# Kernel optimization log

Hardware: AMD Instinct MI355X
Metric: run time of the kernel (lower is better)

## Reference

```python
import jax, jax.numpy as jnp
import numpy as np

N_NODES = 50000
N_EDGES = 1250000
VOCAB = 50000
EMBED = 64
HIDDEN = 64
NUM_REL = 3
N_CLASSES = 2
N_GRAPHS = 512


def setup_inputs() -> dict:
    key = jax.random.key(0)
    ks = jax.random.split(key, 12)
    x = jax.random.randint(ks[0], (N_NODES,), 0, VOCAB, dtype=jnp.int32)
    edge_index = jax.random.randint(ks[1], (2, N_EDGES), 0, N_NODES, dtype=jnp.int32)
    edge_type = jax.random.randint(ks[2], (N_EDGES,), 0, NUM_REL, dtype=jnp.int32)
    batch = jnp.sort(jax.random.randint(ks[3], (N_NODES,), 0, N_GRAPHS, dtype=jnp.int32))
    s = 0.05
    emb = jax.random.normal(ks[4], (VOCAB, EMBED), jnp.float32) * s
    w1_rel = jax.random.normal(ks[5], (NUM_REL, EMBED, HIDDEN), jnp.float32) * s
    w1_root = jax.random.normal(ks[6], (EMBED, HIDDEN), jnp.float32) * s
    b1 = jnp.zeros((HIDDEN,), jnp.float32)
    w2_rel = jax.random.normal(ks[7], (NUM_REL, HIDDEN, HIDDEN), jnp.float32) * s
    w2_root = jax.random.normal(ks[8], (HIDDEN, HIDDEN), jnp.float32) * s
    b2 = jnp.zeros((HIDDEN,), jnp.float32)
    lin_w = jax.random.normal(ks[9], (HIDDEN, N_CLASSES), jnp.float32) * s
    lin_b = jnp.zeros((N_CLASSES,), jnp.float32)
    return {"x": x, "edge_index": edge_index, "edge_type": edge_type, "batch": batch,
            "emb": emb, "w1_rel": w1_rel, "w1_root": w1_root, "b1": b1,
            "w2_rel": w2_rel, "w2_root": w2_root, "b2": b2,
            "lin_w": lin_w, "lin_b": lin_b}


def rgcn_conv(h, src, dst, edge_type, w_rel, w_root, bias):
    # PyG RGCNConv: out = h @ W_root + bias + sum_r mean-aggregated (h_src @ W_r)
    out = h @ w_root + bias
    h_src = h[src]  # [E, F] gather
    for r in range(NUM_REL):
        mask = (edge_type == r).astype(h.dtype)  # [E]
        m = (h_src @ w_rel[r]) * mask[:, None]   # [E, H]
        s = jax.ops.segment_sum(m, dst, num_segments=N_NODES)
        cnt = jax.ops.segment_sum(mask, dst, num_segments=N_NODES)
        out = out + s / jnp.maximum(cnt, 1.0)[:, None]
    return out


def reference(x, edge_index, edge_type, batch, emb, w1_rel, w1_root, b1,
              w2_rel, w2_root, b2, lin_w, lin_b):
    src, dst = edge_index[0], edge_index[1]
    emb_eff = emb.at[0].set(0.0)  # padding_idx=0
    h = emb_eff[x]  # [N, EMBED]
    h = jax.nn.relu(rgcn_conv(h, src, dst, edge_type, w1_rel, w1_root, b1))
    h = jax.nn.relu(rgcn_conv(h, src, dst, edge_type, w2_rel, w2_root, b2))
    # global mean pool over graphs
    sums = jax.ops.segment_sum(h, batch, num_segments=N_GRAPHS)
    cnt = jax.ops.segment_sum(jnp.ones((h.shape[0],), h.dtype), batch, num_segments=N_GRAPHS)
    pooled = sums / jnp.maximum(cnt, 1.0)[:, None]  # [G, HIDDEN]
    return pooled @ lin_w + lin_b  # [G, N_CLASSES]
```

## Files before the change

kernel.cpp:

```cpp
#include <hip/hip_runtime.h>

__global__ __launch_bounds__(256) void embed_kernel(
    const int* __restrict__ x, const float* __restrict__ emb,
    float* __restrict__ h0, int n_nodes)
{
    int t = blockIdx.x * 256 + threadIdx.x;
    if (t >= n_nodes * 16) return;
    int n = t >> 4, q = t & 15;
    int xv = x[n];
    float4 v = {0.f, 0.f, 0.f, 0.f};
    if (xv != 0) v = *(const float4*)(emb + (size_t)xv * 64 + q * 4);
    *(float4*)(h0 + (size_t)n * 64 + q * 4) = v;
}


__global__ __launch_bounds__(256) void bucket_count_kernel(
    const int* __restrict__ ei, int* __restrict__ bucket_count,
    int n_edges, int n_bkt, int per_block)
{
    __shared__ int cnt[512];
    int t = threadIdx.x;
    for (int i = t; i < n_bkt; i += 256) cnt[i] = 0;
    __syncthreads();
    int lo = blockIdx.x * per_block;
    int hi = min(n_edges, lo + per_block);
    for (int e = lo + t; e < hi; e += 256)
        atomicAdd(&cnt[ei[n_edges + e] >> 7], 1);
    __syncthreads();
    for (int i = t; i < n_bkt; i += 256)
        if (cnt[i]) atomicAdd(&bucket_count[i], cnt[i]);
}

__global__ __launch_bounds__(512) void scan_buckets_kernel(
    const int* __restrict__ bucket_count, int* __restrict__ bucket_start,
    int* __restrict__ rowstart, int n_bkt, int n_edges, int n_nodes)
{
    __shared__ int part[512];
    int t = threadIdx.x;
    part[t] = (t < n_bkt) ? bucket_count[t] : 0;
    __syncthreads();
    for (int off = 1; off < 512; off <<= 1) {
        int v = (t >= off) ? part[t - off] : 0;
        __syncthreads();
        part[t] += v;
        __syncthreads();
    }
    if (t == 0) { bucket_start[0] = 0; rowstart[n_nodes] = n_edges; }
    if (t < n_bkt) bucket_start[t + 1] = part[t];
}

__global__ __launch_bounds__(256) void bucket_scatter_kernel(
    const int* __restrict__ ei, const int* __restrict__ et,
    const int* __restrict__ bucket_start, int* __restrict__ bucket_fill,
    int* __restrict__ esort, int n_edges, int n_bkt)
{
    __shared__ int cnt[512], gbase[512], fill2[512];
    const int EPT = 32;
    int t = threadIdx.x;
    int base = blockIdx.x * 256 * EPT;
    for (int i = t; i < n_bkt; i += 256) { cnt[i] = 0; fill2[i] = 0; }
    __syncthreads();
    int pay[EPT], bk[EPT];
#pragma unroll
    for (int i = 0; i < EPT; ++i) {
        int e = base + i * 256 + t;
        bk[i] = -1;
        if (e < n_edges) {
            int s = ei[e], d = ei[n_edges + e], r = et[e];
            int b = d >> 7;
            pay[i] = s | (r << 16) | ((d & 127) << 18);
            bk[i] = b;
            atomicAdd(&cnt[b], 1);
        }
    }
    __syncthreads();
    for (int i = t; i < n_bkt; i += 256)
        if (cnt[i]) gbase[i] = bucket_start[i] + atomicAdd(&bucket_fill[i], cnt[i]);
    __syncthreads();
#pragma unroll
    for (int i = 0; i < EPT; ++i) {
        if (bk[i] >= 0) {
            int pos = gbase[bk[i]] + atomicAdd(&fill2[bk[i]], 1);
            esort[pos] = pay[i];
        }
    }
}

__global__ __launch_bounds__(256) void bucket_sort_kernel(
    const int* __restrict__ bucket_start, int* __restrict__ esort,
    int* __restrict__ scratch, int* __restrict__ rowstart, int n_nodes)
{
    __shared__ int cnt[128], off[128], fill[128], sc[128];
    int t = threadIdx.x, b = blockIdx.x;
    int s = bucket_start[b], e = bucket_start[b + 1];
    if (t < 128) { cnt[t] = 0; fill[t] = 0; }
    __syncthreads();
    int* scr = scratch + (size_t)b * 8192;
    for (int i = s + t; i < e; i += 256) {
        int p = esort[i];
        scr[i - s] = p;
        atomicAdd(&cnt[(p >> 18) & 127], 1);
    }
    __syncthreads();
    if (t < 128) sc[t] = cnt[t];
    __syncthreads();
    for (int o = 1; o < 128; o <<= 1) {
        int v = (t >= o && t < 128) ? sc[t - o] : 0;
        __syncthreads();
        if (t < 128) sc[t] += v;
        __syncthreads();
    }
    if (t < 128) {
        off[t] = sc[t] - cnt[t];
        int d = b * 128 + t;
        if (d < n_nodes) rowstart[d] = s + off[t];
    }
    __syncthreads();
    for (int i = s + t; i < e; i += 256) {
        int p = scr[i - s];
        int dl = (p >> 18) & 127;
        int pos = s + off[dl] + atomicAdd(&fill[dl], 1);
        esort[pos] = p;
    }
}

__global__ __launch_bounds__(256) void agg_kernel(
    const float* __restrict__ hin, const int* __restrict__ rowstart,
    const int* __restrict__ esort, float* __restrict__ means, int n_nodes)
{
    int wid = (blockIdx.x * 256 + threadIdx.x) >> 6;
    int lane = threadIdx.x & 63;
    if (wid >= n_nodes) return;
    int q = lane >> 4;
    int c = lane & 15;
    int s = rowstart[wid], e = rowstart[wid + 1];

    float a0x=0.f,a0y=0.f,a0z=0.f,a0w=0.f, c0=0.f;
    float a1x=0.f,a1y=0.f,a1z=0.f,a1w=0.f, c1=0.f;
    float a2x=0.f,a2y=0.f,a2z=0.f,a2w=0.f, c2=0.f;

    for (int i = s + q; i < e; i += 4) {
        int p = esort[i];
        int src = p & 0xFFFF;
        int r = (p >> 16) & 3;
        float4 v = *(const float4*)(hin + (size_t)src * 64 + c * 4);
        float m0 = (r == 0) ? 1.f : 0.f;
        float m1 = (r == 1) ? 1.f : 0.f;
        float m2 = (r == 2) ? 1.f : 0.f;
        a0x = fmaf(m0, v.x, a0x); a0y = fmaf(m0, v.y, a0y);
        a0z = fmaf(m0, v.z, a0z); a0w = fmaf(m0, v.w, a0w); c0 += m0;
        a1x = fmaf(m1, v.x, a1x); a1y = fmaf(m1, v.y, a1y);
        a1z = fmaf(m1, v.z, a1z); a1w = fmaf(m1, v.w, a1w); c1 += m1;
        a2x = fmaf(m2, v.x, a2x); a2y = fmaf(m2, v.y, a2y);
        a2z = fmaf(m2, v.z, a2z); a2w = fmaf(m2, v.w, a2w); c2 += m2;
    }
#pragma unroll
    for (int off = 16; off < 64; off <<= 1) {
        a0x += __shfl_xor(a0x, off); a0y += __shfl_xor(a0y, off);
        a0z += __shfl_xor(a0z, off); a0w += __shfl_xor(a0w, off);
        a1x += __shfl_xor(a1x, off); a1y += __shfl_xor(a1y, off);
        a1z += __shfl_xor(a1z, off); a1w += __shfl_xor(a1w, off);
        a2x += __shfl_xor(a2x, off); a2y += __shfl_xor(a2y, off);
        a2z += __shfl_xor(a2z, off); a2w += __shfl_xor(a2w, off);
        c0 += __shfl_xor(c0, off); c1 += __shfl_xor(c1, off);
        c2 += __shfl_xor(c2, off);
    }
    if (q < 3) {
        float ax = (q == 0) ? a0x : (q == 1) ? a1x : a2x;
        float ay = (q == 0) ? a0y : (q == 1) ? a1y : a2y;
        float az = (q == 0) ? a0z : (q == 1) ? a1z : a2z;
        float aw = (q == 0) ? a0w : (q == 1) ? a1w : a2w;
        float cc = (q == 0) ? c0  : (q == 1) ? c1  : c2;
        float inv = 1.f / fmaxf(cc, 1.f);
        float4 m;
        m.x = ax * inv; m.y = ay * inv; m.z = az * inv; m.w = aw * inv;
        *(float4*)(means + (size_t)wid * 192 + q * 64 + c * 4) = m;
    }
}

__global__ __launch_bounds__(256) void transform_kernel(
    const float* __restrict__ hin, const float* __restrict__ means,
    const float* __restrict__ wroot, const float* __restrict__ wrel,
    const float* __restrict__ bias, float* __restrict__ hout, int n_nodes)
{
    __shared__ float wsh[256 * 64];
    int t = threadIdx.x;
    {
        const float4* src = (const float4*)wroot;
        float4* dst = (float4*)wsh;
#pragma unroll
        for (int i = 0; i < 4; ++i) dst[t + i * 256] = src[t + i * 256];
        src = (const float4*)wrel;
        dst = (float4*)(wsh + 4096);
#pragma unroll
        for (int i = 0; i < 12; ++i) dst[t + i * 256] = src[t + i * 256];
    }
    __syncthreads();

    int gt = blockIdx.x * 256 + t;
    int g = gt >> 4, q = gt & 15;
    int n0 = g * 4;
    if (n0 >= n_nodes) return;

    float4 b = *(const float4*)(bias + q * 4);
    float acc0x=b.x, acc0y=b.y, acc0z=b.z, acc0w=b.w;
    float acc1x=b.x, acc1y=b.y, acc1z=b.z, acc1w=b.w;
    float acc2x=b.x, acc2y=b.y, acc2z=b.z, acc2w=b.w;
    float acc3x=b.x, acc3y=b.y, acc3z=b.z, acc3w=b.w;

    const float* hv = hin + (size_t)n0 * 64;
#pragma unroll 2
    for (int k4 = 0; k4 < 16; ++k4) {
        float4 va = *(const float4*)(hv +   0 + k4 * 4);
        float4 vb = *(const float4*)(hv +  64 + k4 * 4);
        float4 vc = *(const float4*)(hv + 128 + k4 * 4);
        float4 vd = *(const float4*)(hv + 192 + k4 * 4);
#pragma unroll
        for (int kk = 0; kk < 4; ++kk) {
            float4 w = *(const float4*)(wsh + (k4 * 4 + kk) * 64 + q * 4);
            float a = kk==0?va.x:kk==1?va.y:kk==2?va.z:va.w;
            float bb= kk==0?vb.x:kk==1?vb.y:kk==2?vb.z:vb.w;
            float c = kk==0?vc.x:kk==1?vc.y:kk==2?vc.z:vc.w;
            float d = kk==0?vd.x:kk==1?vd.y:kk==2?vd.z:vd.w;
            acc0x=fmaf(a,w.x,acc0x); acc0y=fmaf(a,w.y,acc0y); acc0z=fmaf(a,w.z,acc0z); acc0w=fmaf(a,w.w,acc0w);
            acc1x=fmaf(bb,w.x,acc1x); acc1y=fmaf(bb,w.y,acc1y); acc1z=fmaf(bb,w.z,acc1z); acc1w=fmaf(bb,w.w,acc1w);
            acc2x=fmaf(c,w.x,acc2x); acc2y=fmaf(c,w.y,acc2y); acc2z=fmaf(c,w.z,acc2z); acc2w=fmaf(c,w.w,acc2w);
            acc3x=fmaf(d,w.x,acc3x); acc3y=fmaf(d,w.y,acc3y); acc3z=fmaf(d,w.z,acc3z); acc3w=fmaf(d,w.w,acc3w);
        }
    }
    const float* mv = means + (size_t)n0 * 192;
#pragma unroll 2
    for (int k4 = 0; k4 < 48; ++k4) {
        float4 va = *(const float4*)(mv +   0 + k4 * 4);
        float4 vb = *(const float4*)(mv + 192 + k4 * 4);
        float4 vc = *(const float4*)(mv + 384 + k4 * 4);
        float4 vd = *(const float4*)(mv + 576 + k4 * 4);
#pragma unroll
        for (int kk = 0; kk < 4; ++kk) {
            float4 w = *(const float4*)(wsh + (64 + k4 * 4 + kk) * 64 + q * 4);
            float a = kk==0?va.x:kk==1?va.y:kk==2?va.z:va.w;
            float bb= kk==0?vb.x:kk==1?vb.y:kk==2?vb.z:vb.w;
            float c = kk==0?vc.x:kk==1?vc.y:kk==2?vc.z:vc.w;
            float d = kk==0?vd.x:kk==1?vd.y:kk==2?vd.z:vd.w;
            acc0x=fmaf(a,w.x,acc0x); acc0y=fmaf(a,w.y,acc0y); acc0z=fmaf(a,w.z,acc0z); acc0w=fmaf(a,w.w,acc0w);
            acc1x=fmaf(bb,w.x,acc1x); acc1y=fmaf(bb,w.y,acc1y); acc1z=fmaf(bb,w.z,acc1z); acc1w=fmaf(bb,w.w,acc1w);
            acc2x=fmaf(c,w.x,acc2x); acc2y=fmaf(c,w.y,acc2y); acc2z=fmaf(c,w.z,acc2z); acc2w=fmaf(c,w.w,acc2w);
            acc3x=fmaf(d,w.x,acc3x); acc3y=fmaf(d,w.y,acc3y); acc3z=fmaf(d,w.z,acc3z); acc3w=fmaf(d,w.w,acc3w);
        }
    }
    float* o = hout + (size_t)n0 * 64 + q * 4;
    float4 r0 = {fmaxf(acc0x,0.f), fmaxf(acc0y,0.f), fmaxf(acc0z,0.f), fmaxf(acc0w,0.f)};
    float4 r1 = {fmaxf(acc1x,0.f), fmaxf(acc1y,0.f), fmaxf(acc1z,0.f), fmaxf(acc1w,0.f)};
    float4 r2 = {fmaxf(acc2x,0.f), fmaxf(acc2y,0.f), fmaxf(acc2z,0.f), fmaxf(acc2w,0.f)};
    float4 r3 = {fmaxf(acc3x,0.f), fmaxf(acc3y,0.f), fmaxf(acc3z,0.f), fmaxf(acc3w,0.f)};
    *(float4*)(o +   0) = r0;
    *(float4*)(o +  64) = r1;
    *(float4*)(o + 128) = r2;
    *(float4*)(o + 192) = r3;
}

__global__ __launch_bounds__(256) void pool_kernel(
    const float* __restrict__ h2, const int* __restrict__ batch,
    const float* __restrict__ linw, const float* __restrict__ linb,
    float* __restrict__ out, int n_nodes, int n_graphs)
{
    int wid = (blockIdx.x * 256 + threadIdx.x) >> 6;
    int lane = threadIdx.x & 63;
    if (wid >= n_graphs) return;
    int g = wid;
    int lo = 0, hi = n_nodes;
    while (lo < hi) { int mid = (lo + hi) >> 1; if (batch[mid] < g) lo = mid + 1; else hi = mid; }
    int s = lo;
    lo = 0; hi = n_nodes;
    while (lo < hi) { int mid = (lo + hi) >> 1; if (batch[mid] < g + 1) lo = mid + 1; else hi = mid; }
    int e = lo;
    float sum = 0.f;
    for (int n = s; n < e; ++n) sum += h2[(size_t)n * 64 + lane];
    float mean = sum / (float)max(e - s, 1);
    float d0 = mean * linw[lane * 2 + 0];
    float d1 = mean * linw[lane * 2 + 1];
    for (int off = 32; off > 0; off >>= 1) {
        d0 += __shfl_down(d0, off);
        d1 += __shfl_down(d1, off);
    }
    if (lane == 0) {
        out[g * 2 + 0] = d0 + linb[0];
        out[g * 2 + 1] = d1 + linb[1];
    }
}

extern "C" void kernel_launch(void* const* d_in, const int* in_sizes, int n_in,
                              void* d_out, int out_size, void* d_ws, size_t ws_size,
                              hipStream_t stream)
{
    const int*   x      = (const int*)d_in[0];
    const int*   ei     = (const int*)d_in[1];
    const int*   et     = (const int*)d_in[2];
    const int*   batch  = (const int*)d_in[3];
    const float* emb    = (const float*)d_in[4];
    const float* w1rel  = (const float*)d_in[5];
    const float* w1root = (const float*)d_in[6];
    const float* b1     = (const float*)d_in[7];
    const float* w2rel  = (const float*)d_in[8];
    const float* w2root = (const float*)d_in[9];
    const float* b2     = (const float*)d_in[10];
    const float* linw   = (const float*)d_in[11];
    const float* linb   = (const float*)d_in[12];
    float* out = (float*)d_out;

    const int N = in_sizes[0];
    const int E = in_sizes[2];
    const int G = out_size / 2;
    const int NBKT = (N + 127) >> 7;

    float* hA        = (float*)d_ws;
    float* hB        = hA + (size_t)N * 64;
    float* means     = hB + (size_t)N * 64;
    int*   esort     = (int*)(means + (size_t)N * 192);
    int*   rowstart  = esort + E;
    int*   bucket_count = rowstart + (N + 1);
    int*   bucket_fill  = bucket_count + 512;
    int*   bucket_start = bucket_fill + 512;

    hipMemsetAsync(bucket_count, 0, (size_t)1024 * sizeof(int), stream);

    embed_kernel<<<(N * 16 + 255) / 256, 256, 0, stream>>>(x, emb, hA, N);

    int per_block = (E + 255) / 256;
    bucket_count_kernel<<<256, 256, 0, stream>>>(ei, bucket_count, E, NBKT, per_block);
    scan_buckets_kernel<<<1, 512, 0, stream>>>(bucket_count, bucket_start, rowstart, NBKT, E, N);
    bucket_scatter_kernel<<<(E + 8191) / 8192, 256, 0, stream>>>(ei, et, bucket_start, bucket_fill, esort, E, NBKT);
    bucket_sort_kernel<<<NBKT, 256, 0, stream>>>(bucket_start, esort, (int*)means, rowstart, N);

    int aggBlocks = (N * 64 + 255) / 256;
    int tfBlocks  = ((N + 3) / 4 * 16 + 255) / 256;
    agg_kernel<<<aggBlocks, 256, 0, stream>>>(hA, rowstart, esort, means, N);
    transform_kernel<<<tfBlocks, 256, 0, stream>>>(hA, means, w1root, w1rel, b1, hB, N);
    agg_kernel<<<aggBlocks, 256, 0, stream>>>(hB, rowstart, esort, means, N);
    transform_kernel<<<tfBlocks, 256, 0, stream>>>(hB, means, w2root, w2rel, b2, hA, N);

    pool_kernel<<<(G * 64 + 255) / 256, 256, 0, stream>>>(hA, batch, linw, linb, out, N, G);
}
```

Baseline: 360.7 us.

## Sort edges by (dst, relation) and tile transform over eight nodes

```diff
diff --git a/kernel.cpp b/kernel.cpp
--- a/kernel.cpp
+++ b/kernel.cpp
@@ -33,7 +33,7 @@
 
 __global__ __launch_bounds__(512) void scan_buckets_kernel(
     const int* __restrict__ bucket_count, int* __restrict__ bucket_start,
-    int* __restrict__ rowstart, int n_bkt, int n_edges, int n_nodes)
+    int* __restrict__ rowstartR, int n_bkt, int n_edges, int n_nodes)
 {
     __shared__ int part[512];
     int t = threadIdx.x;
@@ -45,7 +45,7 @@
         part[t] += v;
         __syncthreads();
     }
-    if (t == 0) { bucket_start[0] = 0; rowstart[n_nodes] = n_edges; }
+    if (t == 0) { bucket_start[0] = 0; rowstartR[4 * n_nodes] = n_edges; }
     if (t < n_bkt) bucket_start[t + 1] = part[t];
 }
 
@@ -88,44 +88,48 @@
 
 __global__ __launch_bounds__(256) void bucket_sort_kernel(
     const int* __restrict__ bucket_start, int* __restrict__ esort,
-    int* __restrict__ scratch, int* __restrict__ rowstart, int n_nodes)
-{
-    __shared__ int cnt[128], off[128], fill[128], sc[128];
+    int* __restrict__ scratch, int* __restrict__ rowstartR, int n_nodes)
+{
+    __shared__ int cnt[512], off[512], fill[512], ps[256];
     int t = threadIdx.x, b = blockIdx.x;
     int s = bucket_start[b], e = bucket_start[b + 1];
-    if (t < 128) { cnt[t] = 0; fill[t] = 0; }
+    cnt[t] = 0; cnt[t + 256] = 0; fill[t] = 0; fill[t + 256] = 0;
     __syncthreads();
     int* scr = scratch + (size_t)b * 8192;
     for (int i = s + t; i < e; i += 256) {
         int p = esort[i];
         scr[i - s] = p;
-        atomicAdd(&cnt[(p >> 18) & 127], 1);
-    }
-    __syncthreads();
-    if (t < 128) sc[t] = cnt[t];
-    __syncthreads();
-    for (int o = 1; o < 128; o <<= 1) {
-        int v = (t >= o && t < 128) ? sc[t - o] : 0;
+        atomicAdd(&cnt[(p >> 16) & 0x1FF], 1);
+    }
+    __syncthreads();
+    int a0 = cnt[2 * t], a1 = cnt[2 * t + 1];
+    ps[t] = a0 + a1;
+    __syncthreads();
+    for (int o = 1; o < 256; o <<= 1) {
+        int v = (t >= o) ? ps[t - o] : 0;
         __syncthreads();
-        if (t < 128) sc[t] += v;
+        ps[t] += v;
         __syncthreads();
     }
-    if (t < 128) {
-        off[t] = sc[t] - cnt[t];
-        int d = b * 128 + t;
-        if (d < n_nodes) rowstart[d] = s + off[t];
-    }
+    int basex = (t > 0) ? ps[t - 1] : 0;
+    off[2 * t] = basex;
+    off[2 * t + 1] = basex + a0;
+    __syncthreads();
+    int d0 = b * 128 + (2 * t >> 2);
+    if (d0 < n_nodes) rowstartR[b * 512 + 2 * t] = s + off[2 * t];
+    int d1 = b * 128 + ((2 * t + 1) >> 2);
+    if (d1 < n_nodes) rowstartR[b * 512 + 2 * t + 1] = s + off[2 * t + 1];
     __syncthreads();
     for (int i = s + t; i < e; i += 256) {
         int p = scr[i - s];
-        int dl = (p >> 18) & 127;
-        int pos = s + off[dl] + atomicAdd(&fill[dl], 1);
+        int bin = (p >> 16) & 0x1FF;
+        int pos = s + off[bin] + atomicAdd(&fill[bin], 1);
         esort[pos] = p;
     }
 }
 
 __global__ __launch_bounds__(256) void agg_kernel(
-    const float* __restrict__ hin, const int* __restrict__ rowstart,
+    const float* __restrict__ hin, const int* __restrict__ rowstartR,
     const int* __restrict__ esort, float* __restrict__ means, int n_nodes)
 {
     int wid = (blockIdx.x * 256 + threadIdx.x) >> 6;
@@ -133,48 +137,27 @@
     if (wid >= n_nodes) return;
     int q = lane >> 4;
     int c = lane & 15;
-    int s = rowstart[wid], e = rowstart[wid + 1];
-
-    float a0x=0.f,a0y=0.f,a0z=0.f,a0w=0.f, c0=0.f;
-    float a1x=0.f,a1y=0.f,a1z=0.f,a1w=0.f, c1=0.f;
-    float a2x=0.f,a2y=0.f,a2z=0.f,a2w=0.f, c2=0.f;
-
-    for (int i = s + q; i < e; i += 4) {
-        int p = esort[i];
-        int src = p & 0xFFFF;
-        int r = (p >> 16) & 3;
-        float4 v = *(const float4*)(hin + (size_t)src * 64 + c * 4);
-        float m0 = (r == 0) ? 1.f : 0.f;
-        float m1 = (r == 1) ? 1.f : 0.f;
-        float m2 = (r == 2) ? 1.f : 0.f;
-        a0x = fmaf(m0, v.x, a0x); a0y = fmaf(m0, v.y, a0y);
-        a0z = fmaf(m0, v.z, a0z); a0w = fmaf(m0, v.w, a0w); c0 += m0;
-        a1x = fmaf(m1, v.x, a1x); a1y = fmaf(m1, v.y, a1y);
-        a1z = fmaf(m1, v.z, a1z); a1w = fmaf(m1, v.w, a1w); c1 += m1;
-        a2x = fmaf(m2, v.x, a2x); a2y = fmaf(m2, v.y, a2y);
-        a2z = fmaf(m2, v.z, a2z); a2w = fmaf(m2, v.w, a2w); c2 += m2;
-    }
-#pragma unroll
-    for (int off = 16; off < 64; off <<= 1) {
-        a0x += __shfl_xor(a0x, off); a0y += __shfl_xor(a0y, off);
-        a0z += __shfl_xor(a0z, off); a0w += __shfl_xor(a0w, off);
-        a1x += __shfl_xor(a1x, off); a1y += __shfl_xor(a1y, off);
-        a1z += __shfl_xor(a1z, off); a1w += __shfl_xor(a1w, off);
-        a2x += __shfl_xor(a2x, off); a2y += __shfl_xor(a2y, off);
-        a2z += __shfl_xor(a2z, off); a2w += __shfl_xor(a2w, off);
-        c0 += __shfl_xor(c0, off); c1 += __shfl_xor(c1, off);
-        c2 += __shfl_xor(c2, off);
-    }
-    if (q < 3) {
-        float ax = (q == 0) ? a0x : (q == 1) ? a1x : a2x;
-        float ay = (q == 0) ? a0y : (q == 1) ? a1y : a2y;
-        float az = (q == 0) ? a0z : (q == 1) ? a1z : a2z;
-        float aw = (q == 0) ? a0w : (q == 1) ? a1w : a2w;
-        float cc = (q == 0) ? c0  : (q == 1) ? c1  : c2;
-        float inv = 1.f / fmaxf(cc, 1.f);
-        float4 m;
-        m.x = ax * inv; m.y = ay * inv; m.z = az * inv; m.w = aw * inv;
-        *(float4*)(means + (size_t)wid * 192 + q * 64 + c * 4) = m;
+    int4 rs = *(const int4*)(rowstartR + wid * 4);
+
+#pragma unroll
+    for (int r = 0; r < 3; ++r) {
+        int sR = (r == 0) ? rs.x : (r == 1) ? rs.y : rs.z;
+        int eR = (r == 0) ? rs.y : (r == 1) ? rs.z : rs.w;
+        float4 a = {0.f, 0.f, 0.f, 0.f};
+        for (int i = sR + q; i < eR; i += 4) {
+            int p = esort[i];
+            float4 v = *(const float4*)(hin + (size_t)(p & 0xFFFF) * 64 + c * 4);
+            a.x += v.x; a.y += v.y; a.z += v.z; a.w += v.w;
+        }
+        a.x += __shfl_xor(a.x, 16); a.y += __shfl_xor(a.y, 16);
+        a.z += __shfl_xor(a.z, 16); a.w += __shfl_xor(a.w, 16);
+        a.x += __shfl_xor(a.x, 32); a.y += __shfl_xor(a.y, 32);
+        a.z += __shfl_xor(a.z, 32); a.w += __shfl_xor(a.w, 32);
+        if (q == r) {
+            float inv = 1.f / (float)max(eR - sR, 1);
+            float4 m = {a.x * inv, a.y * inv, a.z * inv, a.w * inv};
+            *(float4*)(means + (size_t)wid * 192 + r * 64 + c * 4) = m;
+        }
     }
 }
 
@@ -199,64 +182,59 @@
 
     int gt = blockIdx.x * 256 + t;
     int g = gt >> 4, q = gt & 15;
-    int n0 = g * 4;
+    int n0 = g * 8;
     if (n0 >= n_nodes) return;
 
     float4 b = *(const float4*)(bias + q * 4);
-    float acc0x=b.x, acc0y=b.y, acc0z=b.z, acc0w=b.w;
-    float acc1x=b.x, acc1y=b.y, acc1z=b.z, acc1w=b.w;
-    float acc2x=b.x, acc2y=b.y, acc2z=b.z, acc2w=b.w;
-    float acc3x=b.x, acc3y=b.y, acc3z=b.z, acc3w=b.w;
+    float4 acc[8];
+#pragma unroll
+    for (int i = 0; i < 8; ++i) acc[i] = b;
 
     const float* hv = hin + (size_t)n0 * 64;
 #pragma unroll 2
     for (int k4 = 0; k4 < 16; ++k4) {
-        float4 va = *(const float4*)(hv +   0 + k4 * 4);
-        float4 vb = *(const float4*)(hv +  64 + k4 * 4);
-        float4 vc = *(const float4*)(hv + 128 + k4 * 4);
-        float4 vd = *(const float4*)(hv + 192 + k4 * 4);
+        float4 v[8];
+#pragma unroll
+        for (int i = 0; i < 8; ++i) v[i] = *(const float4*)(hv + i * 64 + k4 * 4);
 #pragma unroll
         for (int kk = 0; kk < 4; ++kk) {
             float4 w = *(const float4*)(wsh + (k4 * 4 + kk) * 64 + q * 4);
-            float a = kk==0?va.x:kk==1?va.y:kk==2?va.z:va.w;
-            float bb= kk==0?vb.x:kk==1?vb.y:kk==2?vb.z:vb.w;
-            float c = kk==0?vc.x:kk==1?vc.y:kk==2?vc.z:vc.w;
-            float d = kk==0?vd.x:kk==1?vd.y:kk==2?vd.z:vd.w;
-            acc0x=fmaf(a,w.x,acc0x); acc0y=fmaf(a,w.y,acc0y); acc0z=fmaf(a,w.z,acc0z); acc0w=fmaf(a,w.w,acc0w);
-            acc1x=fmaf(bb,w.x,acc1x); acc1y=fmaf(bb,w.y,acc1y); acc1z=fmaf(bb,w.z,acc1z); acc1w=fmaf(bb,w.w,acc1w);
-            acc2x=fmaf(c,w.x,acc2x); acc2y=fmaf(c,w.y,acc2y); acc2z=fmaf(c,w.z,acc2z); acc2w=fmaf(c,w.w,acc2w);
-            acc3x=fmaf(d,w.x,acc3x); acc3y=fmaf(d,w.y,acc3y); acc3z=fmaf(d,w.z,acc3z); acc3w=fmaf(d,w.w,acc3w);
+#pragma unroll
+            for (int i = 0; i < 8; ++i) {
+                float s = kk == 0 ? v[i].x : kk == 1 ? v[i].y : kk == 2 ? v[i].z : v[i].w;
+                acc[i].x = fmaf(s, w.x, acc[i].x);
+                acc[i].y = fmaf(s, w.y, acc[i].y);
+                acc[i].z = fmaf(s, w.z, acc[i].z);
+                acc[i].w = fmaf(s, w.w, acc[i].w);
+            }
         }
     }
     const float* mv = means + (size_t)n0 * 192;
 #pragma unroll 2
     for (int k4 = 0; k4 < 48; ++k4) {
-        float4 va = *(const float4*)(mv +   0 + k4 * 4);
-        float4 vb = *(const float4*)(mv + 192 + k4 * 4);
-        float4 vc = *(const float4*)(mv + 384 + k4 * 4);
-        float4 vd = *(const float4*)(mv + 576 + k4 * 4);
+        float4 v[8];
+#pragma unroll
+        for (int i = 0; i < 8; ++i) v[i] = *(const float4*)(mv + i * 192 + k4 * 4);
 #pragma unroll
         for (int kk = 0; kk < 4; ++kk) {
             float4 w = *(const float4*)(wsh + (64 + k4 * 4 + kk) * 64 + q * 4);
-            float a = kk==0?va.x:kk==1?va.y:kk==2?va.z:va.w;
-            float bb= kk==0?vb.x:kk==1?vb.y:kk==2?vb.z:vb.w;
-            float c = kk==0?vc.x:kk==1?vc.y:kk==2?vc.z:vc.w;
-            float d = kk==0?vd.x:kk==1?vd.y:kk==2?vd.z:vd.w;
-            acc0x=fmaf(a,w.x,acc0x); acc0y=fmaf(a,w.y,acc0y); acc0z=fmaf(a,w.z,acc0z); acc0w=fmaf(a,w.w,acc0w);
-            acc1x=fmaf(bb,w.x,acc1x); acc1y=fmaf(bb,w.y,acc1y); acc1z=fmaf(bb,w.z,acc1z); acc1w=fmaf(bb,w.w,acc1w);
-            acc2x=fmaf(c,w.x,acc2x); acc2y=fmaf(c,w.y,acc2y); acc2z=fmaf(c,w.z,acc2z); acc2w=fmaf(c,w.w,acc2w);
-            acc3x=fmaf(d,w.x,acc3x); acc3y=fmaf(d,w.y,acc3y); acc3z=fmaf(d,w.z,acc3z); acc3w=fmaf(d,w.w,acc3w);
+#pragma unroll
+            for (int i = 0; i < 8; ++i) {
+                float s = kk == 0 ? v[i].x : kk == 1 ? v[i].y : kk == 2 ? v[i].z : v[i].w;
+                acc[i].x = fmaf(s, w.x, acc[i].x);
+                acc[i].y = fmaf(s, w.y, acc[i].y);
+                acc[i].z = fmaf(s, w.z, acc[i].z);
+                acc[i].w = fmaf(s, w.w, acc[i].w);
+            }
         }
     }
     float* o = hout + (size_t)n0 * 64 + q * 4;
-    float4 r0 = {fmaxf(acc0x,0.f), fmaxf(acc0y,0.f), fmaxf(acc0z,0.f), fmaxf(acc0w,0.f)};
-    float4 r1 = {fmaxf(acc1x,0.f), fmaxf(acc1y,0.f), fmaxf(acc1z,0.f), fmaxf(acc1w,0.f)};
-    float4 r2 = {fmaxf(acc2x,0.f), fmaxf(acc2y,0.f), fmaxf(acc2z,0.f), fmaxf(acc2w,0.f)};
-    float4 r3 = {fmaxf(acc3x,0.f), fmaxf(acc3y,0.f), fmaxf(acc3z,0.f), fmaxf(acc3w,0.f)};
-    *(float4*)(o +   0) = r0;
-    *(float4*)(o +  64) = r1;
-    *(float4*)(o + 128) = r2;
-    *(float4*)(o + 192) = r3;
+#pragma unroll
+    for (int i = 0; i < 8; ++i) {
+        float4 r = {fmaxf(acc[i].x, 0.f), fmaxf(acc[i].y, 0.f),
+                    fmaxf(acc[i].z, 0.f), fmaxf(acc[i].w, 0.f)};
+        *(float4*)(o + i * 64) = r;
+    }
 }
 
 __global__ __launch_bounds__(256) void pool_kernel(
@@ -317,8 +295,8 @@
     float* hB        = hA + (size_t)N * 64;
     float* means     = hB + (size_t)N * 64;
     int*   esort     = (int*)(means + (size_t)N * 192);
-    int*   rowstart  = esort + E;
-    int*   bucket_count = rowstart + (N + 1);
+    int*   rowstartR = esort + E;
+    int*   bucket_count = rowstartR + 4 * N + 4;
     int*   bucket_fill  = bucket_count + 512;
     int*   bucket_start = bucket_fill + 512;
 
@@ -328,15 +306,15 @@
 
     int per_block = (E + 255) / 256;
     bucket_count_kernel<<<256, 256, 0, stream>>>(ei, bucket_count, E, NBKT, per_block);
-    scan_buckets_kernel<<<1, 512, 0, stream>>>(bucket_count, bucket_start, rowstart, NBKT, E, N);
+    scan_buckets_kernel<<<1, 512, 0, stream>>>(bucket_count, bucket_start, rowstartR, NBKT, E, N);
     bucket_scatter_kernel<<<(E + 8191) / 8192, 256, 0, stream>>>(ei, et, bucket_start, bucket_fill, esort, E, NBKT);
-    bucket_sort_kernel<<<NBKT, 256, 0, stream>>>(bucket_start, esort, (int*)means, rowstart, N);
+    bucket_sort_kernel<<<NBKT, 256, 0, stream>>>(bucket_start, esort, (int*)means, rowstartR, N);
 
     int aggBlocks = (N * 64 + 255) / 256;
-    int tfBlocks  = ((N + 3) / 4 * 16 + 255) / 256;
-    agg_kernel<<<aggBlocks, 256, 0, stream>>>(hA, rowstart, esort, means, N);
+    int tfBlocks  = ((N + 7) / 8 * 16 + 255) / 256;
+    agg_kernel<<<aggBlocks, 256, 0, stream>>>(hA, rowstartR, esort, means, N);
     transform_kernel<<<tfBlocks, 256, 0, stream>>>(hA, means, w1root, w1rel, b1, hB, N);
-    agg_kernel<<<aggBlocks, 256, 0, stream>>>(hB, rowstart, esort, means, N);
+    agg_kernel<<<aggBlocks, 256, 0, stream>>>(hB, rowstartR, esort, means, N);
     transform_kernel<<<tfBlocks, 256, 0, stream>>>(hB, means, w2root, w2rel, b2, hA, N);
 
     pool_kernel<<<(G * 64 + 255) / 256, 256, 0, stream>>>(hA, batch, linw, linb, out, N, G);
```

Result: slower. 372.4 us (+3.2%).
